# Performance work log

Measured on AMD Instinct MI355X. Metric: run time of the kernel, lower is better.

The kernel has to match this reference:

```python
import jax, jax.numpy as jnp
import numpy as np

B, T, D = 4, 4096, 2048
NE = 64
TOP_K = 8


def setup_inputs() -> dict:
    key = jax.random.key(0)
    k1, k2 = jax.random.split(key)
    x = jax.random.normal(k1, (B, T, D), dtype=jnp.float32)
    w = jax.random.normal(k2, (NE, D), dtype=jnp.float32) * (1.0 / np.sqrt(D))
    gate_b = jnp.zeros((NE,), dtype=jnp.float32)
    return {"x": x, "w": w, "gate_b": gate_b, "top_k": TOP_K}


def reference(x, w, gate_b, top_k):
    # router logits: [b, t, ne]
    logits = jnp.einsum('nd,btd->btn', w, x)
    scores = jax.nn.sigmoid(logits) + gate_b
    weights, indices = jax.lax.top_k(scores, top_k)
    weights = weights / weights.sum(-1, keepdims=True)
    return (weights, indices, scores)
```

## Files before the change

kernel.cpp:

```cpp
#include <hip/hip_runtime.h>
#include <math.h>

#define D_DIM 2048
#define NE    64
#define NTOK  16384
#define TK    8
#define TOKB  64
#define KS    8
#define KD    (D_DIM / KS)
#define KCH   16
#define NCH   (KD / KCH)
#define BT    512

#define XS_BUF_FLOATS (KS * TOKB * KCH)
#define RED_ROW       72
#define POOL_FLOATS   (KS * TOKB * RED_ROW)

#define OUT_I_OFF (NTOK * TK)
#define OUT_S_OFF (2 * NTOK * TK)

#define GLOBAL_AS __attribute__((address_space(1)))
#define LDS_AS    __attribute__((address_space(3)))

static __device__ __forceinline__ void async_copy16(const float* g, float* l) {
    __builtin_amdgcn_global_load_lds((const GLOBAL_AS void*)g, (LDS_AS void*)l, 16, 0, 0);
}

__global__ __launch_bounds__(BT, 2) void gate_gemm(const float* __restrict__ x,
                                                   const float* __restrict__ w,
                                                   const float* __restrict__ gb,
                                                   float* __restrict__ scores) {
    __shared__ __align__(16) float pool[POOL_FLOATS];

    const int tid  = threadIdx.x;
    const int lane = tid & 63;
    const int ks   = tid >> 6;
    const int lt   = lane >> 3;
    const int le   = lane & 7;
    const int tok0 = blockIdx.x * TOKB;
    const int lt3  = lt & 3;

    const float4* wp[8];
#pragma unroll
    for (int j = 0; j < 8; ++j)
        wp[j] = (const float4*)(w + (size_t)(j * 8 + le) * D_DIM + ks * KD);

    const float* srcb[4];
#pragma unroll
    for (int k = 0; k < 4; ++k) {
        int qq  = tid + k * BT;
        int kss = qq >> 8;
        int r   = qq & 255;
        int ts  = r >> 2;
        int s   = r & 3;
        int dqs = s ^ (ts & 3);
        srcb[k] = x + (size_t)(tok0 + ts) * D_DIM + kss * KD + dqs * 4;
    }

    auto stage = [&](int c, int buf) {
        float* dst = pool + buf * XS_BUF_FLOATS + tid * 4;
#pragma unroll
        for (int k = 0; k < 4; ++k)
            async_copy16(srcb[k] + c * KCH, dst + k * (BT * 4));
    };

    float acc[8][8];
#pragma unroll
    for (int i = 0; i < 8; ++i)
#pragma unroll
        for (int j = 0; j < 8; ++j) acc[i][j] = 0.f;

    float4 wa[8], wb[8];
#pragma unroll
    for (int j = 0; j < 8; ++j) wa[j] = wp[j][0];
    stage(0, 0);

    auto step = [&](float4 (&WC)[8], float4 (&WN)[8], int c, int dq) {
        const int c4n = (c * 4 + dq + 1) & 63;
#pragma unroll
        for (int j = 0; j < 8; ++j) WN[j] = wp[j][c4n];
        const float* xb = pool + (c & 1) * XS_BUF_FLOATS + ks * (TOKB * KCH)
                        + lt * KCH + ((dq ^ lt3) << 2);
        float4 xi[8];
#pragma unroll
        for (int i = 0; i < 8; ++i)
            xi[i] = *(const float4*)(xb + i * (8 * KCH));
#pragma unroll
        for (int i = 0; i < 8; ++i) {
#pragma unroll
            for (int j = 0; j < 8; ++j) {
                acc[i][j] = fmaf(xi[i].x, WC[j].x, acc[i][j]);
                acc[i][j] = fmaf(xi[i].y, WC[j].y, acc[i][j]);
                acc[i][j] = fmaf(xi[i].z, WC[j].z, acc[i][j]);
                acc[i][j] = fmaf(xi[i].w, WC[j].w, acc[i][j]);
            }
        }
    };

    for (int c = 0; c < NCH; ++c) {
        __syncthreads();
        if (c + 1 < NCH) stage(c + 1, (c + 1) & 1);
        step(wa, wb, c, 0);
        step(wb, wa, c, 1);
        step(wa, wb, c, 2);
        step(wb, wa, c, 3);
    }

    __syncthreads();
    {
        const int rb = ks * (TOKB * RED_ROW);
#pragma unroll
        for (int i = 0; i < 8; ++i)
#pragma unroll
            for (int j = 0; j < 8; ++j)
                pool[rb + (i * 8 + lt) * RED_ROW + j * 8 + le] = acc[i][j];
    }
    __syncthreads();
    {
        const int t = tid >> 3;
        const int q = tid & 7;
        float s[8];
#pragma unroll
        for (int u = 0; u < 8; ++u) s[u] = 0.f;
#pragma unroll
        for (int k = 0; k < KS; ++k) {
            const float* rp = pool + k * (TOKB * RED_ROW) + t * RED_ROW + q * 8;
            float4 a = *(const float4*)rp;
            float4 b = *(const float4*)(rp + 4);
            s[0] += a.x; s[1] += a.y; s[2] += a.z; s[3] += a.w;
            s[4] += b.x; s[5] += b.y; s[6] += b.z; s[7] += b.w;
        }
        float4 g0 = *(const float4*)(gb + q * 8);
        float4 g1 = *(const float4*)(gb + q * 8 + 4);
        float r[8];
        r[0] = 1.f / (1.f + expf(-s[0])) + g0.x;
        r[1] = 1.f / (1.f + expf(-s[1])) + g0.y;
        r[2] = 1.f / (1.f + expf(-s[2])) + g0.z;
        r[3] = 1.f / (1.f + expf(-s[3])) + g0.w;
        r[4] = 1.f / (1.f + expf(-s[4])) + g1.x;
        r[5] = 1.f / (1.f + expf(-s[5])) + g1.y;
        r[6] = 1.f / (1.f + expf(-s[6])) + g1.z;
        r[7] = 1.f / (1.f + expf(-s[7])) + g1.w;
        float* so = scores + (size_t)(tok0 + t) * NE + q * 8;
        float4 v0 = {r[0], r[1], r[2], r[3]};
        float4 v1 = {r[4], r[5], r[6], r[7]};
        ((float4*)so)[0] = v0;
        ((float4*)so)[1] = v1;
    }
}

__global__ __launch_bounds__(256) void topk_kernel(const float* __restrict__ scores,
                                                   float* __restrict__ out) {
    const int tid = threadIdx.x;
    const int t   = blockIdx.x * 64 + (tid >> 2);
    const int q   = tid & 3;
    float v[16];
    const float4* sp = (const float4*)(scores + (size_t)t * NE + q * 16);
    float4 a = sp[0], b = sp[1], c = sp[2], d = sp[3];
    v[0] = a.x;  v[1] = a.y;  v[2] = a.z;  v[3] = a.w;
    v[4] = b.x;  v[5] = b.y;  v[6] = b.z;  v[7] = b.w;
    v[8] = c.x;  v[9] = c.y;  v[10] = c.z; v[11] = c.w;
    v[12] = d.x; v[13] = d.y; v[14] = d.z; v[15] = d.w;

    float kv[TK]; int ki[TK];
#pragma unroll
    for (int k = 0; k < TK; ++k) {
        float bv = v[0]; int bi = q * 16;
#pragma unroll
        for (int j = 1; j < 16; ++j) {
            bool gt = v[j] > bv;
            bv = gt ? v[j] : bv;
            bi = gt ? (q * 16 + j) : bi;
        }
#pragma unroll
        for (int off = 1; off < 4; off <<= 1) {
            float ov = __shfl_xor(bv, off);
            int   oi = __shfl_xor(bi, off);
            bool take = (ov > bv) || (ov == bv && oi < bi);
            bv = take ? ov : bv;
            bi = take ? oi : bi;
        }
        int lj = bi - q * 16;
#pragma unroll
        for (int j = 0; j < 16; ++j) v[j] = (j == lj) ? -3e38f : v[j];
        kv[k] = bv; ki[k] = bi;
    }

    if (q == 0) {
        float s = 0.f;
#pragma unroll
        for (int k = 0; k < TK; ++k) s += kv[k];
        float inv = 1.f / s;
        float* ow = out + (size_t)t * TK;
        float* oi = out + OUT_I_OFF + (size_t)t * TK;
#pragma unroll
        for (int k = 0; k < TK; ++k) {
            ow[k] = kv[k] * inv;
            oi[k] = (float)ki[k];
        }
    }
}

extern "C" void kernel_launch(void* const* d_in, const int* in_sizes, int n_in,
                              void* d_out, int out_size, void* d_ws, size_t ws_size,
                              hipStream_t stream) {
    const float* x  = (const float*)d_in[0];
    const float* w  = (const float*)d_in[1];
    const float* gb = (const float*)d_in[2];
    float* out    = (float*)d_out;
    float* scores = out + OUT_S_OFF;
    (void)in_sizes; (void)n_in; (void)out_size; (void)d_ws; (void)ws_size;

    gate_gemm<<<dim3(NTOK / TOKB), dim3(BT), 0, stream>>>(x, w, gb, scores);
    topk_kernel<<<dim3(NTOK / 64), dim3(256), 0, stream>>>(scores, out);
}
```

Measured before the change: 320.6 us.

## Fuse top-k into gate GEMM and shrink token tile for higher occupancy

Merges the separate top-k kernel into the gate GEMM kernel: scores are staged in LDS and the top-8 selection and normalization run in the same block, which removes a launch and the global round trip of the scores. The token tile drops from 64 to 32 and the K chunk grows from 16 to 32, with launch bounds raised to four blocks per CU. The next-chunk async stage is issued after two steps instead of before the first. Per-thread accumulators halve to cut register pressure, but each W load now feeds fewer FMAs, and only 128 of 512 threads do the top-k work.

```diff
diff --git a/kernel.cpp b/kernel.cpp
--- a/kernel.cpp
+++ b/kernel.cpp
@@ -5,16 +5,16 @@
 #define NE    64
 #define NTOK  16384
 #define TK    8
-#define TOKB  64
+#define TOKB  32
 #define KS    8
 #define KD    (D_DIM / KS)
-#define KCH   16
+#define KCH   32
 #define NCH   (KD / KCH)
 #define BT    512
 
-#define XS_BUF_FLOATS (KS * TOKB * KCH)
-#define RED_ROW       72
-#define POOL_FLOATS   (KS * TOKB * RED_ROW)
+#define XSF   (KS * TOKB * KCH)
+#define RROW  72
+#define POOLF (KS * TOKB * RROW)
 
 #define OUT_I_OFF (NTOK * TK)
 #define OUT_S_OFF (2 * NTOK * TK)
@@ -26,47 +26,44 @@
     __builtin_amdgcn_global_load_lds((const GLOBAL_AS void*)g, (LDS_AS void*)l, 16, 0, 0);
 }
 
-__global__ __launch_bounds__(BT, 2) void gate_gemm(const float* __restrict__ x,
-                                                   const float* __restrict__ w,
-                                                   const float* __restrict__ gb,
-                                                   float* __restrict__ scores) {
-    __shared__ __align__(16) float pool[POOL_FLOATS];
-
+__global__ __launch_bounds__(BT, 4) void gate_fused(const float* __restrict__ x,
+                                                    const float* __restrict__ w,
+                                                    const float* __restrict__ gb,
+                                                    float* __restrict__ out) {
+    __shared__ __align__(16) float pool[POOLF];
+
+    float* scores = out + OUT_S_OFF;
     const int tid  = threadIdx.x;
     const int lane = tid & 63;
     const int ks   = tid >> 6;
     const int lt   = lane >> 3;
     const int le   = lane & 7;
     const int tok0 = blockIdx.x * TOKB;
-    const int lt3  = lt & 3;
 
     const float4* wp[8];
 #pragma unroll
     for (int j = 0; j < 8; ++j)
-        wp[j] = (const float4*)(w + (size_t)(j * 8 + le) * D_DIM + ks * KD);
-
-    const float* srcb[4];
-#pragma unroll
-    for (int k = 0; k < 4; ++k) {
-        int qq  = tid + k * BT;
-        int kss = qq >> 8;
-        int r   = qq & 255;
-        int ts  = r >> 2;
-        int s   = r & 3;
-        int dqs = s ^ (ts & 3);
-        srcb[k] = x + (size_t)(tok0 + ts) * D_DIM + kss * KD + dqs * 4;
-    }
+        wp[j] = (const float4*)w + (size_t)(j * 8 + le) * (D_DIM / 4) + ks * (KD / 4);
+
+    const int ks0 = tid >> 8;
+    const int tt  = (tid & 255) >> 3;
+    const int qp  = tid & 7;
+    const int dq0 = qp ^ (tt & 7);
+    const float* srcq[4];
+#pragma unroll
+    for (int k = 0; k < 4; ++k)
+        srcq[k] = x + (size_t)(tok0 + tt) * D_DIM + (ks0 + 2 * k) * KD + dq0 * 4;
 
     auto stage = [&](int c, int buf) {
-        float* dst = pool + buf * XS_BUF_FLOATS + tid * 4;
+        float* d = pool + buf * XSF + tid * 4;
 #pragma unroll
         for (int k = 0; k < 4; ++k)
-            async_copy16(srcb[k] + c * KCH, dst + k * (BT * 4));
+            async_copy16(srcq[k] + c * KCH, d + k * 2048);
     };
 
-    float acc[8][8];
-#pragma unroll
-    for (int i = 0; i < 8; ++i)
+    float acc[4][8];
+#pragma unroll
+    for (int i = 0; i < 4; ++i)
 #pragma unroll
         for (int j = 0; j < 8; ++j) acc[i][j] = 0.f;
 
@@ -75,18 +72,15 @@
     for (int j = 0; j < 8; ++j) wa[j] = wp[j][0];
     stage(0, 0);
 
-    auto step = [&](float4 (&WC)[8], float4 (&WN)[8], int c, int dq) {
-        const int c4n = (c * 4 + dq + 1) & 63;
+    auto step = [&](float4 (&WC)[8], float4 (&WN)[8], const float* xs, int c4n, int dq) {
 #pragma unroll
         for (int j = 0; j < 8; ++j) WN[j] = wp[j][c4n];
-        const float* xb = pool + (c & 1) * XS_BUF_FLOATS + ks * (TOKB * KCH)
-                        + lt * KCH + ((dq ^ lt3) << 2);
-        float4 xi[8];
-#pragma unroll
-        for (int i = 0; i < 8; ++i)
-            xi[i] = *(const float4*)(xb + i * (8 * KCH));
-#pragma unroll
-        for (int i = 0; i < 8; ++i) {
+        const float* xb = xs + ((dq ^ lt) << 2);
+        float4 xi[4];
+#pragma unroll
+        for (int i = 0; i < 4; ++i) xi[i] = *(const float4*)(xb + i * 256);
+#pragma unroll
+        for (int i = 0; i < 4; ++i) {
 #pragma unroll
             for (int j = 0; j < 8; ++j) {
                 acc[i][j] = fmaf(xi[i].x, WC[j].x, acc[i][j]);
@@ -99,104 +93,104 @@
 
     for (int c = 0; c < NCH; ++c) {
         __syncthreads();
+        const float* xs = pool + (c & 1) * XSF + ks * (TOKB * KCH) + lt * KCH;
+        const int cb = c * 8;
+        step(wa, wb, xs, (cb + 1) & 63, 0);
+        step(wb, wa, xs, (cb + 2) & 63, 1);
         if (c + 1 < NCH) stage(c + 1, (c + 1) & 1);
-        step(wa, wb, c, 0);
-        step(wb, wa, c, 1);
-        step(wa, wb, c, 2);
-        step(wb, wa, c, 3);
+        step(wa, wb, xs, (cb + 3) & 63, 2);
+        step(wb, wa, xs, (cb + 4) & 63, 3);
+        step(wa, wb, xs, (cb + 5) & 63, 4);
+        step(wb, wa, xs, (cb + 6) & 63, 5);
+        step(wa, wb, xs, (cb + 7) & 63, 6);
+        step(wb, wa, xs, (cb + 8) & 63, 7);
     }
 
     __syncthreads();
     {
-        const int rb = ks * (TOKB * RED_ROW);
-#pragma unroll
-        for (int i = 0; i < 8; ++i)
+        const int rb = ks * (TOKB * RROW);
+#pragma unroll
+        for (int i = 0; i < 4; ++i)
 #pragma unroll
             for (int j = 0; j < 8; ++j)
-                pool[rb + (i * 8 + lt) * RED_ROW + j * 8 + le] = acc[i][j];
-    }
-    __syncthreads();
+                pool[rb + (i * 8 + lt) * RROW + j * 8 + le] = acc[i][j];
+    }
+    __syncthreads();
+    float sc4[4];
     {
-        const int t = tid >> 3;
-        const int q = tid & 7;
-        float s[8];
-#pragma unroll
-        for (int u = 0; u < 8; ++u) s[u] = 0.f;
+        const int t = tid >> 4;
+        const int q = tid & 15;
+        float4 s = {0.f, 0.f, 0.f, 0.f};
 #pragma unroll
         for (int k = 0; k < KS; ++k) {
-            const float* rp = pool + k * (TOKB * RED_ROW) + t * RED_ROW + q * 8;
-            float4 a = *(const float4*)rp;
-            float4 b = *(const float4*)(rp + 4);
-            s[0] += a.x; s[1] += a.y; s[2] += a.z; s[3] += a.w;
-            s[4] += b.x; s[5] += b.y; s[6] += b.z; s[7] += b.w;
-        }
-        float4 g0 = *(const float4*)(gb + q * 8);
-        float4 g1 = *(const float4*)(gb + q * 8 + 4);
-        float r[8];
-        r[0] = 1.f / (1.f + expf(-s[0])) + g0.x;
-        r[1] = 1.f / (1.f + expf(-s[1])) + g0.y;
-        r[2] = 1.f / (1.f + expf(-s[2])) + g0.z;
-        r[3] = 1.f / (1.f + expf(-s[3])) + g0.w;
-        r[4] = 1.f / (1.f + expf(-s[4])) + g1.x;
-        r[5] = 1.f / (1.f + expf(-s[5])) + g1.y;
-        r[6] = 1.f / (1.f + expf(-s[6])) + g1.z;
-        r[7] = 1.f / (1.f + expf(-s[7])) + g1.w;
-        float* so = scores + (size_t)(tok0 + t) * NE + q * 8;
-        float4 v0 = {r[0], r[1], r[2], r[3]};
-        float4 v1 = {r[4], r[5], r[6], r[7]};
-        ((float4*)so)[0] = v0;
-        ((float4*)so)[1] = v1;
-    }
-}
-
-__global__ __launch_bounds__(256) void topk_kernel(const float* __restrict__ scores,
-                                                   float* __restrict__ out) {
-    const int tid = threadIdx.x;
-    const int t   = blockIdx.x * 64 + (tid >> 2);
-    const int q   = tid & 3;
-    float v[16];
-    const float4* sp = (const float4*)(scores + (size_t)t * NE + q * 16);
-    float4 a = sp[0], b = sp[1], c = sp[2], d = sp[3];
-    v[0] = a.x;  v[1] = a.y;  v[2] = a.z;  v[3] = a.w;
-    v[4] = b.x;  v[5] = b.y;  v[6] = b.z;  v[7] = b.w;
-    v[8] = c.x;  v[9] = c.y;  v[10] = c.z; v[11] = c.w;
-    v[12] = d.x; v[13] = d.y; v[14] = d.z; v[15] = d.w;
-
-    float kv[TK]; int ki[TK];
-#pragma unroll
-    for (int k = 0; k < TK; ++k) {
-        float bv = v[0]; int bi = q * 16;
-#pragma unroll
-        for (int j = 1; j < 16; ++j) {
-            bool gt = v[j] > bv;
-            bv = gt ? v[j] : bv;
-            bi = gt ? (q * 16 + j) : bi;
-        }
-#pragma unroll
-        for (int off = 1; off < 4; off <<= 1) {
-            float ov = __shfl_xor(bv, off);
-            int   oi = __shfl_xor(bi, off);
-            bool take = (ov > bv) || (ov == bv && oi < bi);
-            bv = take ? ov : bv;
-            bi = take ? oi : bi;
-        }
-        int lj = bi - q * 16;
-#pragma unroll
-        for (int j = 0; j < 16; ++j) v[j] = (j == lj) ? -3e38f : v[j];
-        kv[k] = bv; ki[k] = bi;
-    }
-
-    if (q == 0) {
-        float s = 0.f;
-#pragma unroll
-        for (int k = 0; k < TK; ++k) s += kv[k];
-        float inv = 1.f / s;
-        float* ow = out + (size_t)t * TK;
-        float* oi = out + OUT_I_OFF + (size_t)t * TK;
+            float4 a = *(const float4*)(pool + k * (TOKB * RROW) + t * RROW + q * 4);
+            s.x += a.x; s.y += a.y; s.z += a.z; s.w += a.w;
+        }
+        float4 g = *(const float4*)(gb + q * 4);
+        sc4[0] = 1.f / (1.f + expf(-s.x)) + g.x;
+        sc4[1] = 1.f / (1.f + expf(-s.y)) + g.y;
+        sc4[2] = 1.f / (1.f + expf(-s.z)) + g.z;
+        sc4[3] = 1.f / (1.f + expf(-s.w)) + g.w;
+        float* so = scores + (size_t)(tok0 + t) * NE + q * 4;
+        float4 v = {sc4[0], sc4[1], sc4[2], sc4[3]};
+        *(float4*)so = v;
+    }
+    __syncthreads();
+    {
+        const int t = tid >> 4;
+        const int q = tid & 15;
+        float4 v = {sc4[0], sc4[1], sc4[2], sc4[3]};
+        *(float4*)(pool + t * NE + q * 4) = v;
+    }
+    __syncthreads();
+
+    if (tid < 128) {
+        const int t  = tid >> 2;
+        const int q4 = tid & 3;
+        float v[16];
+        const float4* sp = (const float4*)(pool + t * NE + q4 * 16);
+        float4 a = sp[0], b = sp[1], c = sp[2], d = sp[3];
+        v[0] = a.x;  v[1] = a.y;  v[2] = a.z;  v[3] = a.w;
+        v[4] = b.x;  v[5] = b.y;  v[6] = b.z;  v[7] = b.w;
+        v[8] = c.x;  v[9] = c.y;  v[10] = c.z; v[11] = c.w;
+        v[12] = d.x; v[13] = d.y; v[14] = d.z; v[15] = d.w;
+
+        float kv[TK]; int ki[TK];
 #pragma unroll
         for (int k = 0; k < TK; ++k) {
-            ow[k] = kv[k] * inv;
-            oi[k] = (float)ki[k];
+            float bv = v[0]; int bi = q4 * 16;
+#pragma unroll
+            for (int j = 1; j < 16; ++j) {
+                bool gt = v[j] > bv;
+                bv = gt ? v[j] : bv;
+                bi = gt ? (q4 * 16 + j) : bi;
+            }
+#pragma unroll
+            for (int off = 1; off < 4; off <<= 1) {
+                float ov = __shfl_xor(bv, off);
+                int   oi = __shfl_xor(bi, off);
+                bool take = (ov > bv) || (ov == bv && oi < bi);
+                bv = take ? ov : bv;
+                bi = take ? oi : bi;
+            }
+            int lj = bi - q4 * 16;
+#pragma unroll
+            for (int j = 0; j < 16; ++j) v[j] = (j == lj) ? -3e38f : v[j];
+            kv[k] = bv; ki[k] = bi;
+        }
+
+        if (q4 == 0) {
+            float s = 0.f;
+#pragma unroll
+            for (int k = 0; k < TK; ++k) s += kv[k];
+            float inv = 1.f / s;
+            float* ow = out + (size_t)(tok0 + t) * TK;
+            float* oi = out + OUT_I_OFF + (size_t)(tok0 + t) * TK;
+#pragma unroll
+            for (int k = 0; k < TK; ++k) {
+                ow[k] = kv[k] * inv;
+                oi[k] = (float)ki[k];
+            }
         }
     }
 }
@@ -207,10 +201,8 @@
     const float* x  = (const float*)d_in[0];
     const float* w  = (const float*)d_in[1];
     const float* gb = (const float*)d_in[2];
-    float* out    = (float*)d_out;
-    float* scores = out + OUT_S_OFF;
+    float* out = (float*)d_out;
     (void)in_sizes; (void)n_in; (void)out_size; (void)d_ws; (void)ws_size;
 
-    gate_gemm<<<dim3(NTOK / TOKB), dim3(BT), 0, stream>>>(x, w, gb, scores);
-    topk_kernel<<<dim3(NTOK / 64), dim3(256), 0, stream>>>(scores, out);
+    gate_fused<<<dim3(NTOK / TOKB), dim3(BT), 0, stream>>>(x, w, gb, out);
 }
```

Measured after the change: 573.0 us. +78.7%, slower.
